# Optimization experiments

Measured on AMD Instinct MI355X. Metric: run time of the kernel, lower is better.

Reference implementation:

```python
import jax, jax.numpy as jnp
import numpy as np

DIM = 256
HEADS = 8
DIM_FF = 1024
N = 4096
HEAD_DIM = DIM // HEADS
SCALE = HEAD_DIM ** -0.5


def layer_norm(x, gamma, beta, eps=1e-5):
    mu = jnp.mean(x, axis=-1, keepdims=True)
    var = jnp.var(x, axis=-1, keepdims=True)
    return (x - mu) * jax.lax.rsqrt(var + eps) * gamma + beta


def setup_inputs() -> dict:
    key = jax.random.key(0)
    ks = jax.random.split(key, 8)
    x = jax.random.normal(ks[0], (N, DIM), dtype=jnp.float32)
    adj = jax.random.randint(ks[1], (N, N), 0, 2, dtype=jnp.int32)
    adj = adj.at[jnp.arange(N), jnp.arange(N)].set(1)  # self-loops
    s = 1.0 / np.sqrt(DIM)
    w_qkv = jax.random.normal(ks[2], (DIM, 3 * DIM), dtype=jnp.float32) * s
    w_proj = jax.random.normal(ks[3], (DIM, DIM), dtype=jnp.float32) * s
    b_proj = jnp.zeros((DIM,), jnp.float32)
    w1 = jax.random.normal(ks[4], (DIM, DIM_FF), dtype=jnp.float32) * s
    b1 = jnp.zeros((DIM_FF,), jnp.float32)
    w2 = jax.random.normal(ks[5], (DIM_FF, DIM), dtype=jnp.float32) / np.sqrt(DIM_FF)
    b2 = jnp.zeros((DIM,), jnp.float32)
    g1 = jnp.ones((DIM,), jnp.float32)
    be1 = jnp.zeros((DIM,), jnp.float32)
    g2 = jnp.ones((DIM,), jnp.float32)
    be2 = jnp.zeros((DIM,), jnp.float32)
    return {"x": x, "adj": adj, "w_qkv": w_qkv, "w_proj": w_proj,
            "b_proj": b_proj, "w1": w1, "b1": b1, "w2": w2, "b2": b2,
            "g1": g1, "be1": be1, "g2": g2, "be2": be2}


def reference(x, adj, w_qkv, w_proj, b_proj, w1, b1, w2, b2, g1, be1, g2, be2):
    n = x.shape[0]
    qkv = layer_norm(x, g1, be1) @ w_qkv            # (N, 3*dim)
    qkv = qkv.reshape(n, 3, HEADS, HEAD_DIM)
    q, k, v = qkv[:, 0], qkv[:, 1], qkv[:, 2]       # (N, h, d)
    scores = jnp.einsum('nhd,mhd->hnm', q, k) * SCALE
    mask = (adj != 0)[None, :, :]                    # (1, N, N)
    scores = jnp.where(mask, scores, -jnp.inf)
    attn = jax.nn.softmax(scores, axis=-1)           # (h, N, N)
    out = jnp.einsum('hnm,mhd->nhd', attn, v).reshape(n, DIM)
    x = x + out @ w_proj + b_proj
    h2 = layer_norm(x, g2, be2)
    ff = jax.nn.gelu(h2 @ w1 + b1) @ w2 + b2
    return x + ff
```

## Files before the change

### kernel.cpp

```cpp
#include <hip/hip_runtime.h>
#include <hip/hip_bf16.h>

#define NT 4096
#define DM 256
#define NH 8
#define HD 32
#define DFF 1024

typedef __attribute__((ext_vector_type(8))) short s8v;
typedef __attribute__((ext_vector_type(4))) float f4v;
typedef __attribute__((ext_vector_type(2))) float f2v;
typedef __attribute__((ext_vector_type(16))) float f16v;
typedef __attribute__((ext_vector_type(4))) int i4v;

static __device__ __forceinline__ unsigned short f2b(float f){
  union{float f; unsigned u;} v; v.f=f;
  return (unsigned short)((v.u + 0x7FFFu + ((v.u>>16)&1u))>>16);
}

static __device__ __forceinline__ void gl_lds16(const void* g, void* l){
  __builtin_amdgcn_global_load_lds(
      (const __attribute__((address_space(1))) unsigned int*)g,
      (__attribute__((address_space(3))) unsigned int*)l, 16, 0, 0);
}

__global__ __launch_bounds__(256) void prologue_kernel(
    const float* __restrict__ wqkv, const float* __restrict__ wproj,
    const float* __restrict__ w1, const float* __restrict__ w2,
    unsigned short* __restrict__ wqkvT, unsigned short* __restrict__ wprojT,
    unsigned short* __restrict__ w1T, unsigned short* __restrict__ w2T,
    const float* __restrict__ x, const float* __restrict__ g1,
    const float* __restrict__ be1, unsigned short* __restrict__ h1){
  int bx = blockIdx.x;
  if (bx < 128){
    int t = bx*256 + threadIdx.x;
    const int stride = 128*256;
    for (int i=t;i<768*DM;i+=stride){int n=i>>8,k=i&255; wqkvT[i]=f2b(wqkv[k*768+n]);}
    for (int i=t;i<DM*DM;i+=stride){int n=i>>8,k=i&255; wprojT[i]=f2b(wproj[k*DM+n]);}
    for (int i=t;i<DFF*DM;i+=stride){int n=i>>8,k=i&255; w1T[i]=f2b(w1[k*DFF+n]);}
    for (int i=t;i<DM*DFF;i+=stride){int n=i/DFF,k=i-n*DFF; w2T[i]=f2b(w2[k*DM+n]);}
  } else {
    int wv = threadIdx.x>>6, lane = threadIdx.x&63;
    int rbase = (bx-128)*4 + wv;
    for (int j=0;j<8;j++){
      int row = rbase + j*512;
      float4 v = *(const float4*)(x + row*DM + lane*4);
      float s = v.x+v.y+v.z+v.w;
      float sq = v.x*v.x+v.y*v.y+v.z*v.z+v.w*v.w;
      #pragma unroll
      for (int m=1;m<64;m<<=1){ s += __shfl_xor(s,m); sq += __shfl_xor(sq,m); }
      float mu = s*(1.0f/DM);
      float rs = rsqrtf(sq*(1.0f/DM) - mu*mu + 1e-5f);
      float4 gv = *(const float4*)(g1 + lane*4);
      float4 bv = *(const float4*)(be1 + lane*4);
      ushort4 o;
      o.x = f2b((v.x-mu)*rs*gv.x + bv.x);
      o.y = f2b((v.y-mu)*rs*gv.y + bv.y);
      o.z = f2b((v.z-mu)*rs*gv.z + bv.z);
      o.w = f2b((v.w-mu)*rs*gv.w + bv.w);
      *(ushort4*)(h1 + row*DM + lane*4) = o;
    }
  }
}

template<int KD, int MODE>
__global__ __launch_bounds__(256,4) void gemm24(const unsigned short* __restrict__ A,
            const unsigned short* __restrict__ Wt,
            const int* __restrict__ adj, unsigned long long* __restrict__ mask,
            unsigned short* __restrict__ Qp, unsigned short* __restrict__ Kp,
            unsigned short* __restrict__ Vt){
  int wv = threadIdx.x>>6, lane = threadIdx.x&63;
  if (blockIdx.x >= 3){
    int bxl = (blockIdx.x-3)*128 + blockIdx.y;
    int base = (bxl*4 + wv)*64;
    for (int it=0; it<16; ++it){
      int w0 = base + it*4;
      unsigned long long b0 = __ballot(adj[(long)(w0+0)*64 + lane]!=0);
      unsigned long long b1 = __ballot(adj[(long)(w0+1)*64 + lane]!=0);
      unsigned long long b2 = __ballot(adj[(long)(w0+2)*64 + lane]!=0);
      unsigned long long b3 = __ballot(adj[(long)(w0+3)*64 + lane]!=0);
      if (lane==0){ mask[w0]=b0; mask[w0+1]=b1; mask[w0+2]=b2; mask[w0+3]=b3; }
    }
    return;
  }
  int lo = lane&15, hi = lane>>4;
  int r0 = blockIdx.y*32;
  int cbase = blockIdx.x*256 + wv*16;
  const unsigned short* ar0 = A + (r0+lo)*KD + hi*8;
  const unsigned short* ar1 = ar0 + 16*KD;
  const unsigned short* br0 = Wt + (cbase     +lo)*KD + hi*8;
  const unsigned short* br1 = Wt + (cbase+ 64 +lo)*KD + hi*8;
  const unsigned short* br2 = Wt + (cbase+128 +lo)*KD + hi*8;
  const unsigned short* br3 = Wt + (cbase+192 +lo)*KD + hi*8;
  f4v c00={0,0,0,0},c01={0,0,0,0},c02={0,0,0,0},c03={0,0,0,0};
  f4v c10={0,0,0,0},c11={0,0,0,0},c12={0,0,0,0},c13={0,0,0,0};
  #pragma unroll 2
  for (int k0=0;k0<KD;k0+=32){
    s8v a0 = *(const s8v*)(ar0 + k0);
    s8v a1 = *(const s8v*)(ar1 + k0);
    s8v b0 = *(const s8v*)(br0 + k0);
    s8v b1 = *(const s8v*)(br1 + k0);
    s8v b2 = *(const s8v*)(br2 + k0);
    s8v b3 = *(const s8v*)(br3 + k0);
    c00 = __builtin_amdgcn_mfma_f32_16x16x32_bf16(a0,b0,c00,0,0,0);
    c10 = __builtin_amdgcn_mfma_f32_16x16x32_bf16(a1,b0,c10,0,0,0);
    c01 = __builtin_amdgcn_mfma_f32_16x16x32_bf16(a0,b1,c01,0,0,0);
    c11 = __builtin_amdgcn_mfma_f32_16x16x32_bf16(a1,b1,c11,0,0,0);
    c02 = __builtin_amdgcn_mfma_f32_16x16x32_bf16(a0,b2,c02,0,0,0);
    c12 = __builtin_amdgcn_mfma_f32_16x16x32_bf16(a1,b2,c12,0,0,0);
    c03 = __builtin_amdgcn_mfma_f32_16x16x32_bf16(a0,b3,c03,0,0,0);
    c13 = __builtin_amdgcn_mfma_f32_16x16x32_bf16(a1,b3,c13,0,0,0);
  }
  const float scl2 = (float)(0.17677669529663687 * 1.4426950408889634);
  #pragma unroll
  for (int rt=0;rt<2;rt++){
    f4v e0 = rt? c10:c00, e1 = rt? c11:c01, e2 = rt? c12:c02, e3 = rt? c13:c03;
    int nb = r0 + rt*16 + hi*4;
    #pragma unroll
    for (int jj=0;jj<4;jj++){
      f4v acc = jj==0?e0 : jj==1?e1 : jj==2?e2 : e3;
      int c = cbase + jj*64 + lo;
      int which = c>>8, hd = c&255, hh = hd>>5, d = hd&31;
      #pragma unroll
      for (int r=0;r<4;r++){
        int n = nb + r;
        float val = acc[r];
        if (which==0) Qp[(hh*NT+n)*HD+d]=f2b(val*scl2);
        else if (which==1) Kp[(hh*NT+n)*HD+d]=f2b(val);
        else Vt[(hh*HD+d)*NT+n]=f2b(val);
      }
    }
  }
}

__global__ __launch_bounds__(512,2) void attn_kernel(
    const unsigned short* __restrict__ Q, const unsigned short* __restrict__ K,
    const unsigned short* __restrict__ Vt, const unsigned* __restrict__ mb32,
    unsigned short* __restrict__ out){
  __shared__ float Opart[8][32][34];
  __shared__ float llS[8][32];
  int wv = threadIdx.x>>6, lane = threadIdx.x&63;
  int l31 = lane&31, hi5 = lane>>5;
  int h = blockIdx.x, q0 = blockIdx.y*64;
  const unsigned short* QbA = Q + (h*NT + q0 + l31)*HD + hi5*8;
  const unsigned short* QbB = QbA + 32*HD;
  s8v bqA1 = *(const s8v*)(QbA);
  s8v bqA2 = *(const s8v*)(QbA + 16);
  s8v bqB1 = *(const s8v*)(QbB);
  s8v bqB2 = *(const s8v*)(QbB + 16);
  const unsigned short* Kb = K + h*NT*HD;
  const unsigned short* Vb = Vt + (h*HD + l31)*NT;
  const unsigned* mrowA = mb32 + (q0+l31)*(NT/32) + wv*16;
  const unsigned* mrowB = mrowA + 32*(NT/32);
  const float C0 = -11.541560327111707f;
  const f16v c0v = {C0,C0,C0,C0,C0,C0,C0,C0,C0,C0,C0,C0,C0,C0,C0,C0};
  f2v lacA = {0.f,0.f}, lacB = {0.f,0.f};
  f16v accA = {0,0,0,0,0,0,0,0,0,0,0,0,0,0,0,0};
  f16v accB = {0,0,0,0,0,0,0,0,0,0,0,0,0,0,0,0};
  union SU { f16v v; f2v p[8]; };
  const unsigned short* Kt0 = Kb + (wv*512 + l31)*HD + hi5*8;
  s8v kc1 = *(const s8v*)(Kt0);
  s8v kc2 = *(const s8v*)(Kt0 + 16);
  for (int tg=0; tg<4; tg++){
    i4v mw4A = *(const i4v*)(mrowA + tg*4);
    i4v mw4B = *(const i4v*)(mrowB + tg*4);
    #pragma unroll
    for (int ti=0; ti<4; ti++){
      int t = tg*4 + ti;
      int m0 = wv*512 + t*32;
      const unsigned short* Vtp = Vb + m0 + hi5*8;
      s8v av1 = *(const s8v*)(Vtp);
      s8v av2 = *(const s8v*)(Vtp + 16);
      int tn = (t<15)? t+1 : 15;
      const unsigned short* Ktn = Kb + (wv*512 + tn*32 + l31)*HD + hi5*8;
      s8v kn1 = *(const s8v*)(Ktn);
      s8v kn2 = *(const s8v*)(Ktn + 16);
      SU sa, sb;
      __builtin_amdgcn_s_setprio(1);
      sa.v = __builtin_amdgcn_mfma_f32_32x32x16_bf16(kc1, bqA1, c0v, 0,0,0);
      sa.v = __builtin_amdgcn_mfma_f32_32x32x16_bf16(kc2, bqA2, sa.v, 0,0,0);
      sb.v = __builtin_amdgcn_mfma_f32_32x32x16_bf16(kc1, bqB1, c0v, 0,0,0);
      sb.v = __builtin_amdgcn_mfma_f32_32x32x16_bf16(kc2, bqB2, sb.v, 0,0,0);
      __builtin_amdgcn_s_setprio(0);
      unsigned mwA = ((unsigned)mw4A[ti]) >> (4*hi5);
      unsigned mwB = ((unsigned)mw4B[ti]) >> (4*hi5);
      #pragma unroll
      for (int r=0;r<16;r++){
        int bp = (r&3)+8*(r>>2);
        float pa = __builtin_amdgcn_exp2f(sa.v[r]);
        float pb = __builtin_amdgcn_exp2f(sb.v[r]);
        sa.v[r] = ((mwA >> bp) & 1u) ? pa : 0.0f;
        sb.v[r] = ((mwB >> bp) & 1u) ? pb : 0.0f;
      }
      #pragma unroll
      for (int i=0;i<8;i++){ lacA += sa.p[i]; lacB += sb.p[i]; }
      unsigned a0,a1,a2,a3,a4,a5,a6,a7, b0,b1,b2,b3,b4,b5,b6,b7;
      asm("v_cvt_pk_bf16_f32 %0, %1, %2" : "=v"(a0) : "v"(sa.v[0]),  "v"(sa.v[1]));
      asm("v_cvt_pk_bf16_f32 %0, %1, %2" : "=v"(a1) : "v"(sa.v[2]),  "v"(sa.v[3]));
      asm("v_cvt_pk_bf16_f32 %0, %1, %2" : "=v"(a2) : "v"(sa.v[4]),  "v"(sa.v[5]));
      asm("v_cvt_pk_bf16_f32 %0, %1, %2" : "=v"(a3) : "v"(sa.v[6]),  "v"(sa.v[7]));
      asm("v_cvt_pk_bf16_f32 %0, %1, %2" : "=v"(a4) : "v"(sa.v[8]),  "v"(sa.v[9]));
      asm("v_cvt_pk_bf16_f32 %0, %1, %2" : "=v"(a5) : "v"(sa.v[10]), "v"(sa.v[11]));
      asm("v_cvt_pk_bf16_f32 %0, %1, %2" : "=v"(a6) : "v"(sa.v[12]), "v"(sa.v[13]));
      asm("v_cvt_pk_bf16_f32 %0, %1, %2" : "=v"(a7) : "v"(sa.v[14]), "v"(sa.v[15]));
      asm("v_permlane32_swap_b32 %0, %1" : "+v"(a0), "+v"(a2));
      asm("v_permlane32_swap_b32 %0, %1" : "+v"(a1), "+v"(a3));
      asm("v_permlane32_swap_b32 %0, %1" : "+v"(a4), "+v"(a6));
      asm("v_permlane32_swap_b32 %0, %1" : "+v"(a5), "+v"(a7));
      asm("v_cvt_pk_bf16_f32 %0, %1, %2" : "=v"(b0) : "v"(sb.v[0]),  "v"(sb.v[1]));
      asm("v_cvt_pk_bf16_f32 %0, %1, %2" : "=v"(b1) : "v"(sb.v[2]),  "v"(sb.v[3]));
      asm("v_cvt_pk_bf16_f32 %0, %1, %2" : "=v"(b2) : "v"(sb.v[4]),  "v"(sb.v[5]));
      asm("v_cvt_pk_bf16_f32 %0, %1, %2" : "=v"(b3) : "v"(sb.v[6]),  "v"(sb.v[7]));
      asm("v_cvt_pk_bf16_f32 %0, %1, %2" : "=v"(b4) : "v"(sb.v[8]),  "v"(sb.v[9]));
      asm("v_cvt_pk_bf16_f32 %0, %1, %2" : "=v"(b5) : "v"(sb.v[10]), "v"(sb.v[11]));
      asm("v_cvt_pk_bf16_f32 %0, %1, %2" : "=v"(b6) : "v"(sb.v[12]), "v"(sb.v[13]));
      asm("v_cvt_pk_bf16_f32 %0, %1, %2" : "=v"(b7) : "v"(sb.v[14]), "v"(sb.v[15]));
      asm("v_permlane32_swap_b32 %0, %1" : "+v"(b0), "+v"(b2));
      asm("v_permlane32_swap_b32 %0, %1" : "+v"(b1), "+v"(b3));
      asm("v_permlane32_swap_b32 %0, %1" : "+v"(b4), "+v"(b6));
      asm("v_permlane32_swap_b32 %0, %1" : "+v"(b5), "+v"(b7));
      i4v pA1i = {(int)a0,(int)a1,(int)a2,(int)a3};
      i4v pA2i = {(int)a4,(int)a5,(int)a6,(int)a7};
      i4v pB1i = {(int)b0,(int)b1,(int)b2,(int)b3};
      i4v pB2i = {(int)b4,(int)b5,(int)b6,(int)b7};
      s8v pA1 = __builtin_bit_cast(s8v, pA1i);
      s8v pA2 = __builtin_bit_cast(s8v, pA2i);
      s8v pB1 = __builtin_bit_cast(s8v, pB1i);
      s8v pB2 = __builtin_bit_cast(s8v, pB2i);
      __builtin_amdgcn_s_setprio(1);
      accA = __builtin_amdgcn_mfma_f32_32x32x16_bf16(av1, pA1, accA, 0,0,0);
      accA = __builtin_amdgcn_mfma_f32_32x32x16_bf16(av2, pA2, accA, 0,0,0);
      accB = __builtin_amdgcn_mfma_f32_32x32x16_bf16(av1, pB1, accB, 0,0,0);
      accB = __builtin_amdgcn_mfma_f32_32x32x16_bf16(av2, pB2, accB, 0,0,0);
      __builtin_amdgcn_s_setprio(0);
      kc1 = kn1; kc2 = kn2;
    }
  }
  int tid = threadIdx.x;
  int qq = tid>>4, dd = 2*(tid&15);
  #pragma unroll
  for (int i=0;i<8;i++){
    int d = (2*i&3) + 8*(i>>1) + 4*hi5;
    float2 p2; p2.x = accA[2*i]; p2.y = accA[2*i+1];
    *(float2*)&Opart[wv][l31][d] = p2;
  }
  float lsumA = lacA[0] + lacA[1];
  lsumA += __shfl_xor(lsumA, 32);
  if (hi5==0) llS[wv][l31] = lsumA;
  __syncthreads();
  {
    float L=0.f, o0=0.f, o1=0.f;
    #pragma unroll
    for (int u=0;u<8;u++){
      L  += llS[u][qq];
      o0 += Opart[u][qq][dd];
      o1 += Opart[u][qq][dd+1];
    }
    float inv = 1.0f/L;
    float r0 = o0*inv, r1 = o1*inv;
    unsigned pw;
    asm("v_cvt_pk_bf16_f32 %0, %1, %2" : "=v"(pw) : "v"(r0), "v"(r1));
    *(unsigned*)(out + (q0+qq)*DM + h*HD + dd) = pw;
  }
  __syncthreads();
  #pragma unroll
  for (int i=0;i<8;i++){
    int d = (2*i&3) + 8*(i>>1) + 4*hi5;
    float2 p2; p2.x = accB[2*i]; p2.y = accB[2*i+1];
    *(float2*)&Opart[wv][l31][d] = p2;
  }
  float lsumB = lacB[0] + lacB[1];
  lsumB += __shfl_xor(lsumB, 32);
  if (hi5==0) llS[wv][l31] = lsumB;
  __syncthreads();
  {
    float L=0.f, o0=0.f, o1=0.f;
    #pragma unroll
    for (int u=0;u<8;u++){
      L  += llS[u][qq];
      o0 += Opart[u][qq][dd];
      o1 += Opart[u][qq][dd+1];
    }
    float inv = 1.0f/L;
    float r0 = o0*inv, r1 = o1*inv;
    unsigned pw;
    asm("v_cvt_pk_bf16_f32 %0, %1, %2" : "=v"(pw) : "v"(r0), "v"(r1));
    *(unsigned*)(out + (q0+32+qq)*DM + h*HD + dd) = pw;
  }
}

__global__ __launch_bounds__(512,2) void tail_kernel(
    const unsigned short* __restrict__ ao, const unsigned short* __restrict__ wprojT,
    const float* __restrict__ bproj, const float* __restrict__ x,
    const float* __restrict__ g2, const float* __restrict__ be2,
    const unsigned short* __restrict__ w1T, const float* __restrict__ b1,
    const unsigned short* __restrict__ w2T, const float* __restrict__ b2,
    float* __restrict__ outp){
  __shared__ unsigned short h2L[16][DM];
  __shared__ unsigned short gL[16][DFF];
  __shared__ float Ss[8][16], Sq[8][16];
  __shared__ __align__(16) unsigned char wS[3][32768];
  int wv = threadIdx.x>>6, lane = threadIdx.x&63;
  int lo = lane&15, hi = lane>>4;
  int tid = threadIdx.x;
  int r0 = blockIdx.x*16;
  float t[2][4];

#define STAGE_W1(S_, BUF_)                                                    \
  do { int cb_ = (S_)>>2, kt_ = (S_)&3;                                       \
    _Pragma("unroll")                                                         \
    for (int rr=0; rr<4; ++rr){                                               \
      int col_ = cb_*256 + rr*64 + (tid>>3);                                  \
      int ko_  = (tid&7) ^ (col_&7);                                          \
      gl_lds16(w1T + col_*DM + kt_*64 + ko_*8,                                \
               &wS[BUF_][rr*8192 + tid*16]);                                  \
    } } while(0)

#define STAGE_W2(KT, BUF)                                                     \
  do { _Pragma("unroll")                                                      \
    for (int rr=0; rr<4; ++rr){                                               \
      int col_ = rr*64 + (tid>>3);                                            \
      int ko_  = (tid&7) ^ (col_&7);                                          \
      gl_lds16(w2T + col_*DFF + (KT)*64 + ko_*8,                              \
               &wS[BUF][rr*8192 + tid*16]);                                   \
    } } while(0)

#define STAGE_G(G_)                                                           \
  do { int gg_ = (G_);                                                        \
    if (gg_ < 16) { STAGE_W1(gg_, gg_%3); }                                   \
    else          { STAGE_W2(gg_-16, gg_%3); }                                \
  } while(0)

  STAGE_G(0);
  STAGE_G(1);
  STAGE_G(2);

  float b1r[4][2], b2r[2];
  #pragma unroll
  for (int cb=0; cb<4; ++cb){
    b1r[cb][0] = b1[cb*256 +        wv*16 + lo];
    b1r[cb][1] = b1[cb*256 + 128 +  wv*16 + lo];
  }
  b2r[0] = b2[       wv*16 + lo];
  b2r[1] = b2[128 +  wv*16 + lo];

  {
    const unsigned short* ar  = ao + (r0+lo)*DM + hi*8;
    const unsigned short* pb0 = wprojT + (wv*16     +lo)*DM + hi*8;
    const unsigned short* pb1 = wprojT + (wv*16+128 +lo)*DM + hi*8;
    f4v a0={0,0,0,0}, a1={0,0,0,0};
    #pragma unroll
    for (int k0=0;k0<DM;k0+=32){
      s8v a = *(const s8v*)(ar + k0);
      a0 = __builtin_amdgcn_mfma_f32_16x16x32_bf16(a, *(const s8v*)(pb0+k0), a0,0,0,0);
      a1 = __builtin_amdgcn_mfma_f32_16x16x32_bf16(a, *(const s8v*)(pb1+k0), a1,0,0,0);
    }
    float sr[4]={0,0,0,0}, sq[4]={0,0,0,0};
    #pragma unroll
    for (int jj=0;jj<2;jj++){
      f4v acc = jj? a1 : a0;
      int c = jj*128 + wv*16 + lo;
      float bc = bproj[c];
      #pragma unroll
      for (int r=0;r<4;r++){
        int n = r0 + hi*4 + r;
        float tv = acc[r] + bc + x[n*DM+c];
        t[jj][r] = tv; sr[r] += tv; sq[r] += tv*tv;
      }
    }
    #pragma unroll
    for (int m=1;m<16;m<<=1){
      #pragma unroll
      for (int r=0;r<4;r++){ sr[r]+=__shfl_xor(sr[r],m); sq[r]+=__shfl_xor(sq[r],m); }
    }
    if (lo==0){
      #pragma unroll
      for (int r=0;r<4;r++){ Ss[wv][hi*4+r]=sr[r]; Sq[wv][hi*4+r]=sq[r]; }
    }
    __syncthreads();
    #pragma unroll
    for (int r=0;r<4;r++){
      int nl = hi*4+r;
      float S=0.f, Qs=0.f;
      #pragma unroll
      for (int u=0;u<8;u++){ S += Ss[u][nl]; Qs += Sq[u][nl]; }
      float mu = S*(1.0f/DM);
      float rs = rsqrtf(Qs*(1.0f/DM) - mu*mu + 1e-5f);
      #pragma unroll
      for (int jj=0;jj<2;jj++){
        int c = jj*128 + wv*16 + lo;
        unsigned short hv = f2b((t[jj][r]-mu)*rs*g2[c] + be2[c]);
        int g = c>>3;
        h2L[nl][((g^(nl&7))<<3) + (c&7)] = hv;
      }
    }
  }
  __syncthreads();

  for (int cb=0; cb<4; ++cb){
    f4v f0={0,0,0,0}, f1={0,0,0,0};
    int c0i = wv*16 + lo;
    int c1i = c0i + 128;
    #pragma unroll
    for (int kt=0; kt<4; ++kt){
      int g = cb*4 + kt;
      const unsigned char* bufp = wS[g%3];
      #pragma unroll
      for (int ks=0; ks<2; ++ks){
        int k0 = kt*64 + ks*32;
        s8v a  = *(const s8v*)&h2L[lo][(((hi + (k0>>3)) ^ (lo&7))<<3)];
        s8v bw0 = *(const s8v*)(bufp + c0i*128 + ((((ks*4)+hi) ^ (c0i&7))<<4));
        s8v bw1 = *(const s8v*)(bufp + c1i*128 + ((((ks*4)+hi) ^ (c1i&7))<<4));
        f0 = __builtin_amdgcn_mfma_f32_16x16x32_bf16(a, bw0, f0,0,0,0);
        f1 = __builtin_amdgcn_mfma_f32_16x16x32_bf16(a, bw1, f1,0,0,0);
      }
      asm volatile("" ::: "memory");
      __builtin_amdgcn_s_barrier();
      STAGE_G(g+3);
      if (g < 15){
        asm volatile("s_waitcnt vmcnt(8)" ::: "memory");
        __builtin_amdgcn_s_barrier();
      }
    }
    #pragma unroll
    for (int jj=0;jj<2;jj++){
      f4v acc = jj? f1 : f0;
      int c = cb*256 + jj*128 + wv*16 + lo;
      float bc = b1r[cb][jj];
      #pragma unroll
      for (int r=0;r<4;r++){
        int nl = hi*4+r;
        float xx = acc[r] + bc;
        float x2v = xx*xx;
        float arg = xx*(2.302340531f + 0.102952640f*x2v);
        float e  = __builtin_amdgcn_exp2f(arg);
        float rcp = __builtin_amdgcn_rcpf(e + 1.0f);
        unsigned short gv = f2b(xx - xx*rcp);
        int g = c>>3;
        gL[nl][((g^(nl&7))<<3) + (c&7)] = gv;
      }
    }
  }
  __syncthreads();

  {
    f4v e0={0,0,0,0}, e1={0,0,0,0};
    int c0i = wv*16 + lo;
    int c1i = c0i + 128;
    for (int kt=0; kt<16; ++kt){
      int g = 16 + kt;
      const unsigned char* bufp = wS[g%3];
      #pragma unroll
      for (int ks=0; ks<2; ++ks){
        int k0 = kt*64 + ks*32;
        s8v a = *(const s8v*)&gL[lo][(((hi + (k0>>3)) ^ (lo&7))<<3)];
        s8v bw0 = *(const s8v*)(bufp + c0i*128 + ((((ks*4)+hi) ^ (c0i&7))<<4));
        s8v bw1 = *(const s8v*)(bufp + c1i*128 + ((((ks*4)+hi) ^ (c1i&7))<<4));
        e0 = __builtin_amdgcn_mfma_f32_16x16x32_bf16(a, bw0, e0,0,0,0);
        e1 = __builtin_amdgcn_mfma_f32_16x16x32_bf16(a, bw1, e1,0,0,0);
      }
      asm volatile("" ::: "memory");
      __builtin_amdgcn_s_barrier();
      if (g+3 <= 31) { STAGE_G(g+3); }
      if (g <= 28){
        asm volatile("s_waitcnt vmcnt(8)" ::: "memory");
        __builtin_amdgcn_s_barrier();
      } else if (g == 29){
        asm volatile("s_waitcnt vmcnt(4)" ::: "memory");
        __builtin_amdgcn_s_barrier();
      } else if (g == 30){
        asm volatile("s_waitcnt vmcnt(0)" ::: "memory");
        __builtin_amdgcn_s_barrier();
      }
    }
    #pragma unroll
    for (int jj=0;jj<2;jj++){
      f4v acc = jj? e1 : e0;
      int c = jj*128 + wv*16 + lo;
      float bc = b2r[jj];
      #pragma unroll
      for (int r=0;r<4;r++){
        int n = r0 + hi*4 + r;
        outp[n*DM+c] = acc[r] + bc + t[jj][r];
      }
    }
  }
#undef STAGE_G
#undef STAGE_W1
#undef STAGE_W2
}

extern "C" void kernel_launch(void* const* d_in, const int* in_sizes, int n_in,
                              void* d_out, int out_size, void* d_ws, size_t ws_size,
                              hipStream_t stream){
  const float* x     = (const float*)d_in[0];
  const int*   adj   = (const int*)d_in[1];
  const float* wqkv  = (const float*)d_in[2];
  const float* wproj = (const float*)d_in[3];
  const float* bproj = (const float*)d_in[4];
  const float* w1    = (const float*)d_in[5];
  const float* b1    = (const float*)d_in[6];
  const float* w2    = (const float*)d_in[7];
  const float* b2    = (const float*)d_in[8];
  const float* g1    = (const float*)d_in[9];
  const float* be1   = (const float*)d_in[10];
  const float* g2    = (const float*)d_in[11];
  const float* be2   = (const float*)d_in[12];

  char* ws = (char*)d_ws;
  unsigned short* h1    = (unsigned short*)(ws + (0u<<20));
  unsigned short* Qb    = (unsigned short*)(ws + (2u<<20));
  unsigned short* Kb    = (unsigned short*)(ws + (4u<<20));
  unsigned short* Vt    = (unsigned short*)(ws + (6u<<20));
  unsigned short* ao    = (unsigned short*)(ws + (8u<<20));
  unsigned short* wqkvT = (unsigned short*)(ws + (24u<<20));
  unsigned short* wprojT= (unsigned short*)(ws + (25u<<20));
  unsigned short* w1T   = (unsigned short*)(ws + (26u<<20));
  unsigned short* w2T   = (unsigned short*)(ws + (27u<<20));
  unsigned long long* mbits = (unsigned long long*)(ws + (28u<<20));
  float* outF = (float*)d_out;

  hipLaunchKernelGGL(prologue_kernel, dim3(256), dim3(256), 0, stream,
                     wqkv, wproj, w1, w2, wqkvT, wprojT, w1T, w2T,
                     x, g1, be1, h1);
  hipLaunchKernelGGL((gemm24<256,0>), dim3(11,128), dim3(256), 0, stream,
                     h1, wqkvT, adj, mbits, Qb, Kb, Vt);
  hipLaunchKernelGGL(attn_kernel, dim3(8,64), dim3(512), 0, stream,
                     Qb, Kb, Vt, (const unsigned*)mbits, ao);
  hipLaunchKernelGGL(tail_kernel, dim3(256), dim3(512), 0, stream,
                     ao, wprojT, bproj, x, g2, be2, w1T, b1, w2T, b2, outF);
}
```

Before: 98.11 us.

## Store K and V in MFMA-fragment-tiled layout for contiguous per-lane loads

The QKV projection now writes K and V^T into a tiled layout where each 32-key tile is 1024 contiguous bf16 values, arranged so each lane's 8-element MFMA operand sits at lane*8. The attention kernel then loads K and V fragments as fully coalesced 16-byte-per-lane reads instead of strided row reads (V^T previously had a stride of NT between lanes). The cost is more complex index arithmetic and scattered 2-byte stores in the producer kernel.

```diff
diff --git a/kernel.cpp b/kernel.cpp
--- a/kernel.cpp
+++ b/kernel.cpp
@@ -125,9 +125,16 @@
       for (int r=0;r<4;r++){
         int n = nb + r;
         float val = acc[r];
-        if (which==0) Qp[(hh*NT+n)*HD+d]=f2b(val*scl2);
-        else if (which==1) Kp[(hh*NT+n)*HD+d]=f2b(val);
-        else Vt[(hh*HD+d)*NT+n]=f2b(val);
+        if (which==0){
+          Qp[(hh*NT+n)*HD+d] = f2b(val*scl2);
+        } else if (which==1){
+          int idx = (n>>5)*1024 + (d>>4)*512 + ((((d>>3)&1)<<5) + (n&31))*8 + (d&7);
+          Kp[hh*(NT*HD) + idx] = f2b(val);
+        } else {
+          int kk = n&31;
+          int idx = (n>>5)*1024 + (kk>>4)*512 + ((((kk>>3)&1)<<5) + d)*8 + (kk&7);
+          Vt[hh*(NT*HD) + idx] = f2b(val);
+        }
       }
     }
   }
@@ -148,8 +155,8 @@
   s8v bqA2 = *(const s8v*)(QbA + 16);
   s8v bqB1 = *(const s8v*)(QbB);
   s8v bqB2 = *(const s8v*)(QbB + 16);
-  const unsigned short* Kb = K + h*NT*HD;
-  const unsigned short* Vb = Vt + (h*HD + l31)*NT;
+  const unsigned short* Kb = K  + h*(NT*HD) + lane*8;
+  const unsigned short* Vb = Vt + h*(NT*HD) + lane*8;
   const unsigned* mrowA = mb32 + (q0+l31)*(NT/32) + wv*16;
   const unsigned* mrowB = mrowA + 32*(NT/32);
   const float C0 = -11.541560327111707f;
@@ -158,23 +165,21 @@
   f16v accA = {0,0,0,0,0,0,0,0,0,0,0,0,0,0,0,0};
   f16v accB = {0,0,0,0,0,0,0,0,0,0,0,0,0,0,0,0};
   union SU { f16v v; f2v p[8]; };
-  const unsigned short* Kt0 = Kb + (wv*512 + l31)*HD + hi5*8;
-  s8v kc1 = *(const s8v*)(Kt0);
-  s8v kc2 = *(const s8v*)(Kt0 + 16);
+  s8v kc1 = *(const s8v*)(Kb + (wv*16)*1024);
+  s8v kc2 = *(const s8v*)(Kb + (wv*16)*1024 + 512);
   for (int tg=0; tg<4; tg++){
     i4v mw4A = *(const i4v*)(mrowA + tg*4);
     i4v mw4B = *(const i4v*)(mrowB + tg*4);
     #pragma unroll
     for (int ti=0; ti<4; ti++){
       int t = tg*4 + ti;
-      int m0 = wv*512 + t*32;
-      const unsigned short* Vtp = Vb + m0 + hi5*8;
-      s8v av1 = *(const s8v*)(Vtp);
-      s8v av2 = *(const s8v*)(Vtp + 16);
+      int tl = wv*16 + t;
+      s8v av1 = *(const s8v*)(Vb + tl*1024);
+      s8v av2 = *(const s8v*)(Vb + tl*1024 + 512);
       int tn = (t<15)? t+1 : 15;
-      const unsigned short* Ktn = Kb + (wv*512 + tn*32 + l31)*HD + hi5*8;
+      const unsigned short* Ktn = Kb + (wv*16 + tn)*1024;
       s8v kn1 = *(const s8v*)(Ktn);
-      s8v kn2 = *(const s8v*)(Ktn + 16);
+      s8v kn2 = *(const s8v*)(Ktn + 512);
       SU sa, sb;
       __builtin_amdgcn_s_setprio(1);
       sa.v = __builtin_amdgcn_mfma_f32_32x32x16_bf16(kc1, bqA1, c0v, 0,0,0);
```

After: 95.38 us (median of 2 runs). 1.03x faster.
